# Kernel optimization log

Measured on AMD Instinct MI355X. Metric: run time of the kernel, lower is better.

Reference implementation:

```python
import jax, jax.numpy as jnp
from jax import lax
import numpy as np

GAMMA = 0.1           # softmin temperature (init kwarg gamma)
NORMALIZE = True      # init kwarg normalize
BIG = jnp.float32(1e30)  # stand-in for DBL_MAX boundary (finite to keep grads NaN-free)


def _sq_dist(x, y):
    # x: [b, m, d], y: [b, n, d] -> [b, m, n] squared euclidean distances
    return jnp.sum((x[:, :, None, :] - y[:, None, :, :]) ** 2, axis=-1)


def _softmin3(a, b, c):
    # -gamma * log(exp(-a/g) + exp(-b/g) + exp(-c/g)), numerically stable
    z = jnp.stack([a, b, c], axis=0) * (-1.0 / GAMMA)
    return -GAMMA * jax.nn.logsumexp(z, axis=0)


def _soft_dtw(D):
    # D: [m, n] cost matrix -> scalar soft-DTW value R[m, n]
    m, n = D.shape
    # R row 0: R[0,0]=0, R[0,j]=BIG for j>=1
    init_row = jnp.concatenate([jnp.zeros((1,), D.dtype), jnp.full((n,), BIG, D.dtype)])

    def row_step(prev_row, d_row):
        # prev_row = R[i-1, 0..n]; d_row = D[i-1, 0..n-1]
        up = prev_row[1:]       # R[i-1, j]
        upleft = prev_row[:-1]  # R[i-1, j-1]

        def col_step(left, inp):
            d, u, ul = inp
            r = d + _softmin3(u, ul, left)
            return r, r

        _, row_vals = lax.scan(col_step, BIG, (d_row, up, upleft))
        new_row = jnp.concatenate([jnp.full((1,), BIG, D.dtype), row_vals])
        return new_row, None

    last_row, _ = lax.scan(row_step, init_row, D)
    return last_row[-1]


_soft_dtw_batch = jax.vmap(_soft_dtw)  # [b, m, n] -> [b]


def setup_inputs() -> dict:
    key = jax.random.key(0)
    kx, ky = jax.random.split(key)
    x = jax.random.normal(kx, (64, 256, 8), dtype=jnp.float32)
    y = jax.random.normal(ky, (64, 256, 8), dtype=jnp.float32)
    return {"x": x, "y": y}


def reference(x, y):
    loss_xy = _soft_dtw_batch(_sq_dist(x, y))
    if NORMALIZE:
        loss_xx = _soft_dtw_batch(_sq_dist(x, x))
        loss_yy = _soft_dtw_batch(_sq_dist(y, y))
        total = loss_xy - 0.5 * (loss_xx + loss_yy)
    else:
        total = loss_xy
    return jnp.mean(total)
```

## Files before the change

### kernel.cpp

```cpp
#include <hip/hip_runtime.h>
#include <type_traits>

typedef _Float16 h2 __attribute__((ext_vector_type(2)));

static constexpr float K1   = -14.426950408889634074f;
static constexpr float M2K1 = 28.853900817779268148f;
static constexpr float KOUT = -0.069314718055994530942f;
static constexpr float WBIG = -1.0e30f;

__device__ __forceinline__ float dpp_shr1(float v, float fill) {
    int r = __builtin_amdgcn_update_dpp(__float_as_int(fill), __float_as_int(v),
                                        0x138 , 0xf, 0xf, false);
    return __int_as_float(r);
}

__device__ __forceinline__ unsigned pack2(float a, float b) {
    h2 p; p[0] = (_Float16)a; p[1] = (_Float16)b;
    return __builtin_bit_cast(unsigned, p);
}

__device__ __forceinline__ float hdot(h2 a, h2 b, float c) {
#if __has_builtin(__builtin_amdgcn_fdot2)
    return __builtin_amdgcn_fdot2(a, b, c, false);
#else
    return fmaf((float)a[1], (float)b[1], fmaf((float)a[0], (float)b[0], c));
#endif
}

__global__ void __attribute__((amdgpu_waves_per_eu(1, 1))) __launch_bounds__(64, 1)
sdtw_kernel(const float* __restrict__ x, const float* __restrict__ y,
            float* __restrict__ out)
{
    const int batch = blockIdx.x;
    const int pair  = blockIdx.y;
    const int lane  = threadIdx.x;

    const float* A  = (pair == 2 ? y : x) + batch * 2048;
    const float* Bp = (pair == 1 ? x : y) + batch * 2048;

    __shared__ unsigned xHs[4][256];
    __shared__ float    nxs[256];

    #pragma unroll
    for (int rr = 0; rr < 4; ++rr) {
        int r = lane + rr * 64;
        float4 a0 = *reinterpret_cast<const float4*>(A + r * 8);
        float4 a1 = *reinterpret_cast<const float4*>(A + r * 8 + 4);
        unsigned u0 = pack2(a0.x, a0.y), u1 = pack2(a0.z, a0.w);
        unsigned u2 = pack2(a1.x, a1.y), u3 = pack2(a1.z, a1.w);
        xHs[0][r] = u0; xHs[1][r] = u1; xHs[2][r] = u2; xHs[3][r] = u3;
        h2 h0 = __builtin_bit_cast(h2, u0), h1 = __builtin_bit_cast(h2, u1);
        h2 h2v = __builtin_bit_cast(h2, u2), h3 = __builtin_bit_cast(h2, u3);
        nxs[r] = hdot(h3, h3, hdot(h2v, h2v, hdot(h1, h1, hdot(h0, h0, 0.0f))));
    }

    h2 bh[4][4]; float Knb[4];
    #pragma unroll
    for (int cc = 0; cc < 4; ++cc) {
        const float* bp = Bp + (4 * lane + cc) * 8;
        float4 b0 = *reinterpret_cast<const float4*>(bp);
        float4 b1 = *reinterpret_cast<const float4*>(bp + 4);
        bh[cc][0] = __builtin_bit_cast(h2, pack2(b0.x, b0.y));
        bh[cc][1] = __builtin_bit_cast(h2, pack2(b0.z, b0.w));
        bh[cc][2] = __builtin_bit_cast(h2, pack2(b1.x, b1.y));
        bh[cc][3] = __builtin_bit_cast(h2, pack2(b1.z, b1.w));
        float nb = hdot(bh[cc][3], bh[cc][3], hdot(bh[cc][2], bh[cc][2],
                   hdot(bh[cc][1], bh[cc][1], hdot(bh[cc][0], bh[cc][0], 0.0f))));
        Knb[cc] = K1 * nb;
    }

    __syncthreads();

    float up[4] = {WBIG, WBIG, WBIG, WBIG};
    float own_last  = WBIG;
    float left_prev = (lane == 0) ? 0.0f : WBIG;

    unsigned xc[4], xn[4]; float nxc, nxn;
    xc[0]=xHs[0][0]; xc[1]=xHs[1][0]; xc[2]=xHs[2][0]; xc[3]=xHs[3][0]; nxc=nxs[0];

    auto step = [&](auto phc, int s, unsigned (&XC)[4], float& NXC,
                    unsigned (&XN)[4], float& NXN) {
        constexpr int PH = decltype(phc)::value;
        int ipf = s + 1 - lane;
        ipf = ipf < 0 ? 0 : (ipf > 255 ? 255 : ipf);
        XN[0]=xHs[0][ipf]; XN[1]=xHs[1][ipf]; XN[2]=xHs[2][ipf]; XN[3]=xHs[3][ipf];
        NXN = nxs[ipf];

        float lin  = dpp_shr1(own_last, WBIG);
        float ulin = left_prev;
        left_prev  = lin;

        const int i = s - lane;
        bool act = (PH == 0) ? (i >= 0) : (PH == 2) ? (i < 256) : true;
        if (act) {
            float u0=up[0], u1=up[1], u2=up[2], u3=up[3];
            float ulc = ulin;
            if (PH == 0) {
                if (i == 0) { u0=u1=u2=u3=WBIG; if (lane) ulc = WBIG; }
            }
            const float uu [4] = {u0, u1, u2, u3};
            const float uls[4] = {ulc, u0, u1, u2};

            float knx = K1 * NXC;
            float Dw[4], a2[4], Dwa2[4];
            h2 xv0 = __builtin_bit_cast(h2, XC[0]);
            h2 xv1 = __builtin_bit_cast(h2, XC[1]);
            h2 xv2 = __builtin_bit_cast(h2, XC[2]);
            h2 xv3 = __builtin_bit_cast(h2, XC[3]);
            #pragma unroll
            for (int cc = 0; cc < 4; ++cc) {
                float dot = hdot(xv3, bh[cc][3], hdot(xv2, bh[cc][2],
                            hdot(xv1, bh[cc][1], hdot(xv0, bh[cc][0], 0.0f))));
                Dw[cc] = fmaf(M2K1, dot, knx + Knb[cc]);
            }
            #pragma unroll
            for (int cc = 0; cc < 4; ++cc) {
                float d2 = uu[cc] - uls[cc];
                float m2 = fmaxf(uu[cc], uls[cc]);
                float t  = __builtin_amdgcn_exp2f(-fabsf(d2));
                float a  = m2 + __builtin_amdgcn_logf(1.0f + t);
                a2[cc]   = a;
                Dwa2[cc] = Dw[cc] + a;
            }
            float lft = lin;
            #pragma unroll
            for (int cc = 0; cc < 4; ++cc) {
                float q   = Dw[cc] + lft;
                float dlt = a2[cc] - lft;
                float t2  = __builtin_amdgcn_exp2f(-fabsf(dlt));
                float l2  = __builtin_amdgcn_logf(1.0f + t2);
                float w   = fmaxf(Dwa2[cc], q) + l2;
                up[cc] = w;
                lft    = w;
            }
            own_last = lft;
        }
    };

    std::integral_constant<int,0> P0; std::integral_constant<int,1> P1;
    std::integral_constant<int,2> P2;
    for (int s = 0;   s < 64;  s += 2) { step(P0, s, xc, nxc, xn, nxn); step(P0, s+1, xn, nxn, xc, nxc); }
    for (int s = 64;  s < 256; s += 2) { step(P1, s, xc, nxc, xn, nxn); step(P1, s+1, xn, nxn, xc, nxc); }
    for (int s = 256; s < 320; s += 2) { step(P2, s, xc, nxc, xn, nxn); step(P2, s+1, xn, nxn, xc, nxc); }

    if (lane == 63) {
        float r   = own_last * KOUT;
        float wgt = (pair == 0) ? (1.0f / 64.0f) : (-0.5f / 64.0f);
        atomicAdd(out, r * wgt);
    }
}

extern "C" void kernel_launch(void* const* d_in, const int* in_sizes, int n_in,
                              void* d_out, int out_size, void* d_ws, size_t ws_size,
                              hipStream_t stream)
{
    const float* x = (const float*)d_in[0];
    const float* y = (const float*)d_in[1];
    float* out = (float*)d_out;

    hipMemsetAsync(out, 0, out_size * sizeof(float), stream);
    hipLaunchKernelGGL(sdtw_kernel, dim3(64, 3), dim3(64), 0, stream, x, y, out);
}
```

Baseline: 126.0 us.

## Run soft-DTW recurrence in exp domain with mantissa/exponent split

Switches the DP state from log-domain values to linear probabilities stored as a float mantissa plus an integer exponent. The softmin log-sum-exp becomes ldexp-aligned additions and a multiply by exp2 of the distance term. This takes the per-cell exp2/log transcendentals off the serial left-to-right dependency chain, leaving only one independent exp2 per cell and a single log at the end. In exchange it carries twice the state registers and adds integer max, ldexp and frexp work to each cell, and it relies on a sentinel exponent to stand in for the infinite boundary.

```diff
diff --git a/kernel.cpp b/kernel.cpp
--- a/kernel.cpp
+++ b/kernel.cpp
@@ -6,24 +6,48 @@
 static constexpr float K1   = -14.426950408889634074f;
 static constexpr float M2K1 = 28.853900817779268148f;
 static constexpr float KOUT = -0.069314718055994530942f;
-static constexpr float WBIG = -1.0e30f;
+static constexpr int   SENT = -(1 << 28);
 
-__device__ __forceinline__ float dpp_shr1(float v, float fill) {
+__device__ __forceinline__ float dppf(float v, float fill) {
     int r = __builtin_amdgcn_update_dpp(__float_as_int(fill), __float_as_int(v),
                                         0x138 , 0xf, 0xf, false);
     return __int_as_float(r);
+}
+__device__ __forceinline__ int dppi(int v, int fill) {
+    return __builtin_amdgcn_update_dpp(fill, v, 0x138, 0xf, 0xf, false);
 }
 
 __device__ __forceinline__ unsigned pack2(float a, float b) {
     h2 p; p[0] = (_Float16)a; p[1] = (_Float16)b;
     return __builtin_bit_cast(unsigned, p);
 }
-
 __device__ __forceinline__ float hdot(h2 a, h2 b, float c) {
 #if __has_builtin(__builtin_amdgcn_fdot2)
     return __builtin_amdgcn_fdot2(a, b, c, false);
 #else
     return fmaf((float)a[1], (float)b[1], fmaf((float)a[0], (float)b[0], c));
+#endif
+}
+
+__device__ __forceinline__ float ldx(float x, int n) {
+#if __has_builtin(__builtin_amdgcn_ldexpf)
+    return __builtin_amdgcn_ldexpf(x, n);
+#else
+    return ldexpf(x, n);
+#endif
+}
+__device__ __forceinline__ float fxm(float x) {
+#if __has_builtin(__builtin_amdgcn_frexp_mantf)
+    return __builtin_amdgcn_frexp_mantf(x);
+#else
+    int e; return frexpf(x, &e);
+#endif
+}
+__device__ __forceinline__ int fxe(float x) {
+#if __has_builtin(__builtin_amdgcn_frexp_expf)
+    return __builtin_amdgcn_frexp_expf(x);
+#else
+    int e; frexpf(x, &e); return e;
 #endif
 }
 
@@ -71,9 +95,12 @@
 
     __syncthreads();
 
-    float up[4] = {WBIG, WBIG, WBIG, WBIG};
-    float own_last  = WBIG;
-    float left_prev = (lane == 0) ? 0.0f : WBIG;
+    float Um[4]; int Ue[4];
+    #pragma unroll
+    for (int j = 0; j < 4; ++j) { Um[j] = 0.0f; Ue[j] = SENT; }
+    float ol_m = 0.0f; int ol_e = SENT;
+    float lp_m = (lane == 0) ? 1.0f : 0.0f;
+    int   lp_e = (lane == 0) ? 0    : SENT;
 
     unsigned xc[4], xn[4]; float nxc, nxn;
     xc[0]=xHs[0][0]; xc[1]=xHs[1][0]; xc[2]=xHs[2][0]; xc[3]=xHs[3][0]; nxc=nxs[0];
@@ -86,54 +113,54 @@
         XN[0]=xHs[0][ipf]; XN[1]=xHs[1][ipf]; XN[2]=xHs[2][ipf]; XN[3]=xHs[3][ipf];
         NXN = nxs[ipf];
 
-        float lin  = dpp_shr1(own_last, WBIG);
-        float ulin = left_prev;
-        left_prev  = lin;
+        float lin_m  = dppf(ol_m, 0.0f);  int lin_e  = dppi(ol_e, SENT);
+        float ulin_m = lp_m;              int ulin_e = lp_e;
+        lp_m = lin_m; lp_e = lin_e;
 
         const int i = s - lane;
         bool act = (PH == 0) ? (i >= 0) : (PH == 2) ? (i < 256) : true;
         if (act) {
-            float u0=up[0], u1=up[1], u2=up[2], u3=up[3];
-            float ulc = ulin;
-            if (PH == 0) {
-                if (i == 0) { u0=u1=u2=u3=WBIG; if (lane) ulc = WBIG; }
-            }
-            const float uu [4] = {u0, u1, u2, u3};
-            const float uls[4] = {ulc, u0, u1, u2};
-
             float knx = K1 * NXC;
-            float Dw[4], a2[4], Dwa2[4];
             h2 xv0 = __builtin_bit_cast(h2, XC[0]);
             h2 xv1 = __builtin_bit_cast(h2, XC[1]);
             h2 xv2 = __builtin_bit_cast(h2, XC[2]);
             h2 xv3 = __builtin_bit_cast(h2, XC[3]);
+            float Bm[4]; int Be[4];
             #pragma unroll
             for (int cc = 0; cc < 4; ++cc) {
                 float dot = hdot(xv3, bh[cc][3], hdot(xv2, bh[cc][2],
                             hdot(xv1, bh[cc][1], hdot(xv0, bh[cc][0], 0.0f))));
-                Dw[cc] = fmaf(M2K1, dot, knx + Knb[cc]);
+                float Dw  = fmaf(M2K1, dot, knx + Knb[cc]);
+                float t   = truncf(Dw);
+                Bm[cc] = __builtin_amdgcn_exp2f(Dw - t);
+                Be[cc] = (int)t;
+            }
+            float Am[4]; int Ae[4];
+            {
+                float um1 = ulin_m; int ue1 = ulin_e;
+                #pragma unroll
+                for (int cc = 0; cc < 4; ++cc) {
+                    int pe = (Ue[cc] > ue1) ? Ue[cc] : ue1;
+                    Am[cc] = ldx(Um[cc], Ue[cc] - pe) + ldx(um1, ue1 - pe);
+                    Ae[cc] = pe;
+                    um1 = Um[cc]; ue1 = Ue[cc];
+                }
+            }
+            float Lm = lin_m; int Le = lin_e;
+            float nUm[4]; int nUe[4];
+            #pragma unroll
+            for (int cc = 0; cc < 4; ++cc) {
+                int   em = (Ae[cc] > Le) ? Ae[cc] : Le;
+                float S  = ldx(Am[cc], Ae[cc] - em) + ldx(Lm, Le - em);
+                float Wm = Bm[cc] * S;
+                int   We = Be[cc] + em;
+                nUm[cc] = fxm(Wm);
+                nUe[cc] = We + fxe(Wm);
+                Lm = Wm; Le = We;
             }
             #pragma unroll
-            for (int cc = 0; cc < 4; ++cc) {
-                float d2 = uu[cc] - uls[cc];
-                float m2 = fmaxf(uu[cc], uls[cc]);
-                float t  = __builtin_amdgcn_exp2f(-fabsf(d2));
-                float a  = m2 + __builtin_amdgcn_logf(1.0f + t);
-                a2[cc]   = a;
-                Dwa2[cc] = Dw[cc] + a;
-            }
-            float lft = lin;
-            #pragma unroll
-            for (int cc = 0; cc < 4; ++cc) {
-                float q   = Dw[cc] + lft;
-                float dlt = a2[cc] - lft;
-                float t2  = __builtin_amdgcn_exp2f(-fabsf(dlt));
-                float l2  = __builtin_amdgcn_logf(1.0f + t2);
-                float w   = fmaxf(Dwa2[cc], q) + l2;
-                up[cc] = w;
-                lft    = w;
-            }
-            own_last = lft;
+            for (int cc = 0; cc < 4; ++cc) { Um[cc] = nUm[cc]; Ue[cc] = nUe[cc]; }
+            ol_m = nUm[3]; ol_e = nUe[3];
         }
     };
 
@@ -144,9 +171,9 @@
     for (int s = 256; s < 320; s += 2) { step(P2, s, xc, nxc, xn, nxn); step(P2, s+1, xn, nxn, xc, nxc); }
 
     if (lane == 63) {
-        float r   = own_last * KOUT;
+        float w   = (float)ol_e + __builtin_amdgcn_logf(ol_m);
         float wgt = (pair == 0) ? (1.0f / 64.0f) : (-0.5f / 64.0f);
-        atomicAdd(out, r * wgt);
+        atomicAdd(out, KOUT * w * wgt);
     }
 }
 
```

New measurement: 132.9 us. +5.5%, slower.
